# Performance work log

Hardware: AMD Instinct MI355X
Metric: run time of the kernel (lower is better)

Reference implementation:

```python
import jax, jax.numpy as jnp
import numpy as np
import math

D_MODEL = 1024
N_HEADS = 16
SEQ = 2048
BATCH = 2


def setup_inputs() -> dict:
    key = jax.random.key(0)
    ks = jax.random.split(key, 7)
    scale = 1.0 / math.sqrt(D_MODEL)
    return {
        "q": jax.random.normal(ks[0], (SEQ, BATCH, D_MODEL), jnp.float32),
        "k": jax.random.normal(ks[1], (SEQ, BATCH, D_MODEL), jnp.float32),
        "v": jax.random.normal(ks[2], (SEQ, BATCH, D_MODEL), jnp.float32),
        "in_proj_w": jax.random.normal(ks[3], (3 * D_MODEL, D_MODEL), jnp.float32) * scale,
        "in_proj_b": jax.random.normal(ks[4], (3 * D_MODEL,), jnp.float32) * 0.01,
        "out_proj_w": jax.random.normal(ks[5], (D_MODEL, D_MODEL), jnp.float32) * scale,
        "out_proj_b": jax.random.normal(ks[6], (D_MODEL,), jnp.float32) * 0.01,
    }


def reference(q, k, v, in_proj_w, in_proj_b, out_proj_w, out_proj_b):
    # q, k, v: (S, B, D) seq-first layout as in the torch module
    S, B, D = q.shape
    H = N_HEADS
    dk = D // H
    wq, wk, wv = jnp.split(in_proj_w, 3, axis=0)   # each (D, D)
    bq, bk, bv = jnp.split(in_proj_b, 3, axis=0)   # each (D,)
    qp = q @ wq.T + bq
    kp = k @ wk.T + bk
    vp = v @ wv.T + bv
    # (S, B, D) -> (S, B*H, dk) -> (B*H, S, dk)
    def to_heads(x, s):
        return x.reshape(s, B * H, dk).transpose(1, 0, 2)
    qh = to_heads(qp, S)
    kh = to_heads(kp, k.shape[0])
    vh = to_heads(vp, v.shape[0])
    # scores: (B*H, Sq, Sk)
    scores = jnp.einsum('bqd,bkd->bqk', qh, kh) / math.sqrt(dk)
    probs = jax.nn.softmax(scores, axis=-1)
    attn = jnp.einsum('bqk,bkd->bqd', probs, vh)   # (B*H, S, dk)
    # (B*H, S, dk) -> (S, B*H, dk) -> (S*B, D)
    attn = attn.transpose(1, 0, 2).reshape(S * B, D)
    out = attn @ out_proj_w.T + out_proj_b
    return out.reshape(S, B, D)
```

## Files before the change

kernel.cpp:

```cpp
#include <hip/hip_runtime.h>
#include <math.h>

#define SEQ    2048
#define BATCH  2
#define DMODEL 1024
#define NHEADS 16
#define DK     64

typedef __attribute__((ext_vector_type(8))) short  bf16x8;
typedef __attribute__((ext_vector_type(4))) float  f32x4;
typedef __attribute__((ext_vector_type(8))) unsigned short u16x8;

#define GLD16(gp, lp) __builtin_amdgcn_global_load_lds(                      \
    (__attribute__((address_space(1))) void*)(gp),                            \
    (__attribute__((address_space(3))) void*)(lp), 16, 0, 0)

__device__ inline unsigned short f2bf(float f) {
    unsigned int u = __float_as_uint(f);
    u += 0x7fffu + ((u >> 16) & 1u);
    return (unsigned short)(u >> 16);
}

__device__ inline unsigned int pk2bf(float a, float b) {
#if __has_builtin(__builtin_amdgcn_cvt_pk_bf16_f32)
    typedef __attribute__((ext_vector_type(2))) __bf16 v2bf;
    v2bf r = __builtin_amdgcn_cvt_pk_bf16_f32(a, b);
    unsigned int u; __builtin_memcpy(&u, &r, 4); return u;
#else
    return (unsigned int)f2bf(a) | ((unsigned int)f2bf(b) << 16);
#endif
}

__device__ inline float fast_exp2(float x) {
#if __has_builtin(__builtin_amdgcn_exp2f)
    return __builtin_amdgcn_exp2f(x);
#else
    return __expf(x * 0.69314718055994531f);
#endif
}

#define WS_QB   0u
#define WS_KB   4194304u
#define WS_VB   8388608u
#define WS_WIB  12582912u
#define WS_WOB  15728640u
#define WS_QH   16777216u
#define WS_KH   20971520u
#define WS_VT   25165824u
#define WS_ATT  29360128u

__global__ __launch_bounds__(256) void cast_all_kernel(
    const float* __restrict__ q, const float* __restrict__ k,
    const float* __restrict__ v, const float* __restrict__ w_in,
    const float* __restrict__ w_out, unsigned short* __restrict__ ws)
{
    const int gid = blockIdx.x * 256 + threadIdx.x;
    const float* src; unsigned short* dst;
    if (gid < 524288)       { int g = gid;           src = q     + (size_t)g*8; dst = ws + WS_QB  + (size_t)g*8; }
    else if (gid < 1048576) { int g = gid - 524288;  src = k     + (size_t)g*8; dst = ws + WS_KB  + (size_t)g*8; }
    else if (gid < 1572864) { int g = gid - 1048576; src = v     + (size_t)g*8; dst = ws + WS_VB  + (size_t)g*8; }
    else if (gid < 1966080) { int g = gid - 1572864; src = w_in  + (size_t)g*8; dst = ws + WS_WIB + (size_t)g*8; }
    else                    { int g = gid - 1966080; src = w_out + (size_t)g*8; dst = ws + WS_WOB + (size_t)g*8; }
    float4 a = *(const float4*)src;
    float4 b = *(const float4*)(src + 4);
    u16x8 o;
    o[0]=f2bf(a.x); o[1]=f2bf(a.y); o[2]=f2bf(a.z); o[3]=f2bf(a.w);
    o[4]=f2bf(b.x); o[5]=f2bf(b.y); o[6]=f2bf(b.z); o[7]=f2bf(b.w);
    *(u16x8*)dst = o;
}

__global__ __launch_bounds__(256) void qkv_gemm_kernel(
    const unsigned short* __restrict__ ws_in, const float* __restrict__ bias,
    unsigned short* __restrict__ ws_out)
{
    __shared__ unsigned short As[128*32];
    __shared__ unsigned short Bs[128*32];

    const int t    = threadIdx.x;
    const int lane = t & 63;
    const int w    = t >> 6;
    const int lrow = lane & 15;
    const int quad = lane >> 4;
    const int wm   = (w >> 1) * 64;
    const int wn   = (w & 1) * 64;

    const int n0    = blockIdx.x * 128;
    const int m0    = blockIdx.y * 128;
    const int which = n0 >> 10;

    const unsigned short* A = ws_in + WS_QB + (size_t)which * 4194304u;
    const unsigned short* B = ws_in + WS_WIB;

    const int srow = t >> 2;
    const int scc  = (t & 3) ^ ((t >> 3) & 3);
    const unsigned short* gA0 = A + (size_t)(m0 + srow) * 1024 + scc * 8;
    const unsigned short* gA1 = A + (size_t)(m0 + 64 + srow) * 1024 + scc * 8;
    const unsigned short* gB0 = B + (size_t)(n0 + srow) * 1024 + scc * 8;
    const unsigned short* gB1 = B + (size_t)(n0 + 64 + srow) * 1024 + scc * 8;

    f32x4 acc[4][4] = {};

    #pragma unroll 1
    for (int kt = 0; kt < 1024; kt += 32) {
        __syncthreads();
        GLD16(gA0, As + (size_t)t * 8);
        GLD16(gA1, As + (size_t)(t + 256) * 8);
        GLD16(gB0, Bs + (size_t)t * 8);
        GLD16(gB1, Bs + (size_t)(t + 256) * 8);
        gA0 += 32; gA1 += 32; gB0 += 32; gB1 += 32;
        __syncthreads();

        bf16x8 af[4], bf[4];
        #pragma unroll
        for (int mt = 0; mt < 4; ++mt) {
            const int r = wm + mt*16 + lrow;
            af[mt] = *(const bf16x8*)(As + r*32 + ((quad ^ ((r>>1)&3))*8));
        }
        #pragma unroll
        for (int nt = 0; nt < 4; ++nt) {
            const int r = wn + nt*16 + lrow;
            bf[nt] = *(const bf16x8*)(Bs + r*32 + ((quad ^ ((r>>1)&3))*8));
        }
        #pragma unroll
        for (int mt = 0; mt < 4; ++mt)
            #pragma unroll
            for (int nt = 0; nt < 4; ++nt)
                acc[mt][nt] = __builtin_amdgcn_mfma_f32_16x16x32_bf16(
                    af[mt], bf[nt], acc[mt][nt], 0, 0, 0);
    }

    unsigned short* dstQK = ws_out + WS_QH + (size_t)which * 4194304u;
    unsigned short* dstV  = ws_out + WS_VT;
    const float qscale = 0.18033688011112042f;

    #pragma unroll
    for (int nt = 0; nt < 4; ++nt) {
        const int n = n0 + wn + nt*16 + lrow;
        const float bn = bias[n];
        const int h = (n & 1023) >> 6;
        const int d = n & 63;
        #pragma unroll
        for (int mt = 0; mt < 4; ++mt) {
            if (which < 2) {
                #pragma unroll
                for (int r = 0; r < 4; ++r) {
                    const int m = m0 + wm + mt*16 + quad*4 + r;
                    const int s = m >> 1, b = m & 1;
                    float val = acc[mt][nt][r] + bn;
                    if (which == 0) val *= qscale;
                    dstQK[((size_t)((b<<4) + h) * 2048 + s) * 64 + d] = f2bf(val);
                }
            } else {
                const int m_base = m0 + wm + mt*16 + quad*4;
                const int s0 = m_base >> 1;
                unsigned int pk0 = pk2bf(acc[mt][nt][0] + bn, acc[mt][nt][2] + bn);
                unsigned int pk1 = pk2bf(acc[mt][nt][1] + bn, acc[mt][nt][3] + bn);
                *(unsigned int*)(dstV + ((size_t)h*64 + d)*2048 + s0)        = pk0;
                *(unsigned int*)(dstV + ((size_t)(16 + h)*64 + d)*2048 + s0) = pk1;
            }
        }
    }
}

__global__ __launch_bounds__(128) void attn_mfma_kernel(
    const unsigned short* __restrict__ qh, const unsigned short* __restrict__ kh,
    const unsigned short* __restrict__ vt, unsigned short* __restrict__ attn)
{
    __shared__ unsigned short Qs[64*64];
    __shared__ unsigned short Ks[64*64];
    __shared__ unsigned short Vts[64*64];
    __shared__ unsigned short Ps[64*64];

    const int t    = threadIdx.x;
    const int lane = t & 63;
    const int w    = t >> 6;
    const int lrow = lane & 15;
    const int quad = lane >> 4;

    const int qt = blockIdx.x;
    const int bh = blockIdx.y;

    const unsigned short* Qg = qh + ((size_t)bh * 2048 + qt * 64) * 64;
    const unsigned short* Kb = kh + (size_t)bh * 2048 * 64;
    const unsigned short* Vb = vt + (size_t)bh * 64 * 2048;

    #pragma unroll
    for (int i = 0; i < 4; ++i) {
        const int c = i*128 + t;
        const int row = c >> 3, cc = (c & 7) ^ (row & 7);
        GLD16(Qg + (size_t)row*64 + cc*8, Qs + (size_t)c*8);
    }

    f32x4 O[4][2] = {};
    float m_i[2] = {-INFINITY, -INFINITY}, l_i[2] = {0.f, 0.f};

    #pragma unroll 1
    for (int ktile = 0; ktile < 32; ++ktile) {
        __syncthreads();
        const unsigned short* Kg = Kb + (size_t)ktile * 64 * 64;
        const unsigned short* Vg = Vb + (size_t)ktile * 64;
        #pragma unroll
        for (int i = 0; i < 4; ++i) {
            const int c = i*128 + t;
            const int row = c >> 3, cc = (c & 7) ^ (row & 7);
            GLD16(Kg + (size_t)row*64   + cc*8, Ks  + (size_t)c*8);
            GLD16(Vg + (size_t)row*2048 + cc*8, Vts + (size_t)c*8);
        }
        __syncthreads();

        f32x4 ST[4][2] = {};
        #pragma unroll
        for (int kk = 0; kk < 2; ++kk) {
            bf16x8 kf[4], qf[2];
            #pragma unroll
            for (int m = 0; m < 4; ++m) {
                const int r = m*16 + lrow;
                kf[m] = *(const bf16x8*)(Ks + r*64 + (((kk*4+quad) ^ (r&7))*8));
            }
            #pragma unroll
            for (int n = 0; n < 2; ++n) {
                const int r = w*32 + n*16 + lrow;
                qf[n] = *(const bf16x8*)(Qs + r*64 + (((kk*4+quad) ^ (r&7))*8));
            }
            #pragma unroll
            for (int m = 0; m < 4; ++m)
                #pragma unroll
                for (int n = 0; n < 2; ++n)
                    ST[m][n] = __builtin_amdgcn_mfma_f32_16x16x32_bf16(
                        kf[m], qf[n], ST[m][n], 0, 0, 0);
        }

        float mx[2], al[2];
        int anynew = 0;
        #pragma unroll
        for (int n = 0; n < 2; ++n) {
            float mm;
            #pragma unroll
            for (int m = 0; m < 4; ++m) {
                float m01 = fmaxf(fmaxf(ST[m][n][0], ST[m][n][1]),
                                  fmaxf(ST[m][n][2], ST[m][n][3]));
                mm = (m == 0) ? m01 : fmaxf(mm, m01);
            }
            mm = fmaxf(mm, __shfl_xor(mm, 16, 64));
            mm = fmaxf(mm, __shfl_xor(mm, 32, 64));
            mx[n] = mm;
            anynew |= (mm > m_i[n]);
        }

        if (__any(anynew)) {
            #pragma unroll
            for (int n = 0; n < 2; ++n) {
                const float mn = fmaxf(m_i[n], mx[n]);
                al[n] = fast_exp2(m_i[n] - mn);
                m_i[n] = mn;
            }
            #pragma unroll
            for (int dt = 0; dt < 4; ++dt)
                #pragma unroll
                for (int n = 0; n < 2; ++n)
                    O[dt][n] *= al[n];
        } else {
            al[0] = 1.f; al[1] = 1.f;
        }

        #pragma unroll
        for (int n = 0; n < 2; ++n) {
            const int prow = w*32 + n*16 + lrow;
            const float mn = m_i[n];
            float rsum = 0.f;
            #pragma unroll
            for (int m = 0; m < 4; ++m) {
                const float p0 = fast_exp2(ST[m][n][0] - mn);
                const float p1 = fast_exp2(ST[m][n][1] - mn);
                const float p2 = fast_exp2(ST[m][n][2] - mn);
                const float p3 = fast_exp2(ST[m][n][3] - mn);
                rsum += (p0 + p1) + (p2 + p3);
                uint2 pk;
                pk.x = pk2bf(p0, p1);
                pk.y = pk2bf(p2, p3);
                const int sc = (m*2 + (quad >> 1)) ^ (prow & 7);
                *(uint2*)(Ps + prow*64 + sc*8 + (quad & 1)*4) = pk;
            }
            rsum += __shfl_xor(rsum, 16, 64);
            rsum += __shfl_xor(rsum, 32, 64);
            l_i[n] = l_i[n]*al[n] + rsum;
        }

        #pragma unroll
        for (int kk = 0; kk < 2; ++kk) {
            bf16x8 vf[4], pf[2];
            #pragma unroll
            for (int dt = 0; dt < 4; ++dt) {
                const int r = dt*16 + lrow;
                vf[dt] = *(const bf16x8*)(Vts + r*64 + (((kk*4+quad) ^ (r&7))*8));
            }
            #pragma unroll
            for (int n = 0; n < 2; ++n) {
                const int r = w*32 + n*16 + lrow;
                pf[n] = *(const bf16x8*)(Ps + r*64 + (((kk*4+quad) ^ (r&7))*8));
            }
            #pragma unroll
            for (int dt = 0; dt < 4; ++dt)
                #pragma unroll
                for (int n = 0; n < 2; ++n)
                    O[dt][n] = __builtin_amdgcn_mfma_f32_16x16x32_bf16(
                        vf[dt], pf[n], O[dt][n], 0, 0, 0);
        }
    }

    const int b_ = bh >> 4, h_ = bh & 15;
    #pragma unroll
    for (int n = 0; n < 2; ++n) {
        const float inv = 1.f / l_i[n];
        const int s_ = qt*64 + w*32 + n*16 + lrow;
        unsigned short* dst = attn + ((size_t)(s_*2 + b_)) * 1024 + h_*64;
        #pragma unroll
        for (int dt = 0; dt < 4; ++dt) {
            uint2 pk;
            pk.x = pk2bf(O[dt][n][0]*inv, O[dt][n][1]*inv);
            pk.y = pk2bf(O[dt][n][2]*inv, O[dt][n][3]*inv);
            *(uint2*)(dst + dt*16 + quad*4) = pk;
        }
    }
}

__global__ __launch_bounds__(256) void out_gemm_kernel(
    const unsigned short* __restrict__ A, const unsigned short* __restrict__ B,
    const float* __restrict__ bias, float* __restrict__ out)
{
    __shared__ unsigned short As[64*32];
    __shared__ unsigned short Bs[128*32];

    const int t    = threadIdx.x;
    const int lane = t & 63;
    const int w    = t >> 6;
    const int lrow = lane & 15;
    const int quad = lane >> 4;
    const int wn   = (w >> 1) * 64;
    const int wm   = (w & 1) * 32;

    const int n0 = blockIdx.x * 128;
    const int m0 = blockIdx.y * 64;

    const int srow = t >> 2;
    const int scc  = (t & 3) ^ ((t >> 3) & 3);
    const unsigned short* gA0 = A + (size_t)(m0 + srow) * 1024 + scc * 8;
    const unsigned short* gB0 = B + (size_t)(n0 + srow) * 1024 + scc * 8;
    const unsigned short* gB1 = B + (size_t)(n0 + 64 + srow) * 1024 + scc * 8;

    f32x4 acc[2][4] = {};

    #pragma unroll 1
    for (int kt = 0; kt < 1024; kt += 32) {
        __syncthreads();
        GLD16(gA0, As + (size_t)t * 8);
        GLD16(gB0, Bs + (size_t)t * 8);
        GLD16(gB1, Bs + (size_t)(t + 256) * 8);
        gA0 += 32; gB0 += 32; gB1 += 32;
        __syncthreads();

        bf16x8 af[2], bf[4];
        #pragma unroll
        for (int mt = 0; mt < 2; ++mt) {
            const int r = wm + mt*16 + lrow;
            af[mt] = *(const bf16x8*)(As + r*32 + ((quad ^ ((r>>1)&3))*8));
        }
        #pragma unroll
        for (int nt = 0; nt < 4; ++nt) {
            const int r = wn + nt*16 + lrow;
            bf[nt] = *(const bf16x8*)(Bs + r*32 + ((quad ^ ((r>>1)&3))*8));
        }
        #pragma unroll
        for (int mt = 0; mt < 2; ++mt)
            #pragma unroll
            for (int nt = 0; nt < 4; ++nt)
                acc[mt][nt] = __builtin_amdgcn_mfma_f32_16x16x32_bf16(
                    af[mt], bf[nt], acc[mt][nt], 0, 0, 0);
    }

    #pragma unroll
    for (int nt = 0; nt < 4; ++nt) {
        const int n = n0 + wn + nt*16 + lrow;
        const float bn = bias[n];
        #pragma unroll
        for (int mt = 0; mt < 2; ++mt) {
            #pragma unroll
            for (int r = 0; r < 4; ++r) {
                const int m = m0 + wm + mt*16 + quad*4 + r;
                out[(size_t)m * 1024 + n] = acc[mt][nt][r] + bn;
            }
        }
    }
}

extern "C" void kernel_launch(void* const* d_in, const int* in_sizes, int n_in,
                              void* d_out, int out_size, void* d_ws, size_t ws_size,
                              hipStream_t stream) {
    const float* q     = (const float*)d_in[0];
    const float* k     = (const float*)d_in[1];
    const float* v     = (const float*)d_in[2];
    const float* w_in  = (const float*)d_in[3];
    const float* b_in  = (const float*)d_in[4];
    const float* w_out = (const float*)d_in[5];
    const float* b_out = (const float*)d_in[6];
    float* out = (float*)d_out;

    unsigned short* ws = (unsigned short*)d_ws;

    cast_all_kernel<<<8192, 256, 0, stream>>>(q, k, v, w_in, w_out, ws);
    qkv_gemm_kernel<<<dim3(24, 32), 256, 0, stream>>>(ws, b_in, ws);
    attn_mfma_kernel<<<dim3(32, 32), 128, 0, stream>>>(
        ws + WS_QH, ws + WS_KH, ws + WS_VT, ws + WS_ATT);
    out_gemm_kernel<<<dim3(8, 64), 256, 0, stream>>>(
        ws + WS_ATT, ws + WS_WOB, b_out, out);
}
```

Baseline: 252.4 us.

## Compute softmax row sums via MFMA ones-row and use four waves per block

The attention kernel now launches 256 threads (four waves), each wave owning 16 query rows instead of 32. The shuffle-based row-sum reduction is replaced by an extra V tile row filled with bf16 1.0, so the P·V MFMA also accumulates the softmax denominator in a fifth accumulator. This removes per-tile shuffle reductions and halves per-wave register state, at the cost of one extra MFMA per k-step and lower K/V reuse per wave.

```diff
diff --git a/kernel.cpp b/kernel.cpp
--- a/kernel.cpp
+++ b/kernel.cpp
@@ -162,13 +162,13 @@
     }
 }
 
-__global__ __launch_bounds__(128) void attn_mfma_kernel(
+__global__ __launch_bounds__(256) void attn_mfma_kernel(
     const unsigned short* __restrict__ qh, const unsigned short* __restrict__ kh,
     const unsigned short* __restrict__ vt, unsigned short* __restrict__ attn)
 {
     __shared__ unsigned short Qs[64*64];
     __shared__ unsigned short Ks[64*64];
-    __shared__ unsigned short Vts[64*64];
+    __shared__ unsigned short Vts[80*64];
     __shared__ unsigned short Ps[64*64];
 
     const int t    = threadIdx.x;
@@ -185,14 +185,22 @@
     const unsigned short* Vb = vt + (size_t)bh * 64 * 2048;
 
     #pragma unroll
-    for (int i = 0; i < 4; ++i) {
-        const int c = i*128 + t;
+    for (int i = 0; i < 2; ++i) {
+        const int c = i*256 + t;
         const int row = c >> 3, cc = (c & 7) ^ (row & 7);
         GLD16(Qg + (size_t)row*64 + cc*8, Qs + (size_t)c*8);
     }
-
-    f32x4 O[4][2] = {};
-    float m_i[2] = {-INFINITY, -INFINITY}, l_i[2] = {0.f, 0.f};
+    if (t < 128) {
+        const int row = 64 + (t >> 3);
+        const unsigned short fill = (row == 64) ? (unsigned short)0x3F80 : (unsigned short)0;
+        u16x8 cv;
+        #pragma unroll
+        for (int j = 0; j < 8; ++j) cv[j] = fill;
+        *(u16x8*)(Vts + row*64 + (t & 7)*8) = cv;
+    }
+
+    f32x4 O[5] = {};
+    float m_i = -INFINITY;
 
     #pragma unroll 1
     for (int ktile = 0; ktile < 32; ++ktile) {
@@ -200,127 +208,82 @@
         const unsigned short* Kg = Kb + (size_t)ktile * 64 * 64;
         const unsigned short* Vg = Vb + (size_t)ktile * 64;
         #pragma unroll
-        for (int i = 0; i < 4; ++i) {
-            const int c = i*128 + t;
+        for (int i = 0; i < 2; ++i) {
+            const int c = i*256 + t;
             const int row = c >> 3, cc = (c & 7) ^ (row & 7);
             GLD16(Kg + (size_t)row*64   + cc*8, Ks  + (size_t)c*8);
             GLD16(Vg + (size_t)row*2048 + cc*8, Vts + (size_t)c*8);
         }
         __syncthreads();
 
-        f32x4 ST[4][2] = {};
+        f32x4 ST[4] = {};
         #pragma unroll
         for (int kk = 0; kk < 2; ++kk) {
-            bf16x8 kf[4], qf[2];
+            const int qr = w*16 + lrow;
+            bf16x8 qf = *(const bf16x8*)(Qs + qr*64 + (((kk*4+quad) ^ (qr&7))*8));
             #pragma unroll
             for (int m = 0; m < 4; ++m) {
                 const int r = m*16 + lrow;
-                kf[m] = *(const bf16x8*)(Ks + r*64 + (((kk*4+quad) ^ (r&7))*8));
+                bf16x8 kf = *(const bf16x8*)(Ks + r*64 + (((kk*4+quad) ^ (r&7))*8));
+                ST[m] = __builtin_amdgcn_mfma_f32_16x16x32_bf16(kf, qf, ST[m], 0, 0, 0);
             }
-            #pragma unroll
-            for (int n = 0; n < 2; ++n) {
-                const int r = w*32 + n*16 + lrow;
-                qf[n] = *(const bf16x8*)(Qs + r*64 + (((kk*4+quad) ^ (r&7))*8));
+        }
+
+        float mm = fmaxf(fmaxf(ST[0][0], ST[0][1]), fmaxf(ST[0][2], ST[0][3]));
+        #pragma unroll
+        for (int m = 1; m < 4; ++m)
+            mm = fmaxf(mm, fmaxf(fmaxf(ST[m][0], ST[m][1]),
+                                 fmaxf(ST[m][2], ST[m][3])));
+        mm = fmaxf(mm, __shfl_xor(mm, 16, 64));
+        mm = fmaxf(mm, __shfl_xor(mm, 32, 64));
+
+        if (__any(mm > m_i)) {
+            const float mn = fmaxf(m_i, mm);
+            const float al = fast_exp2(m_i - mn);
+            m_i = mn;
+            #pragma unroll
+            for (int d = 0; d < 5; ++d) O[d] *= al;
+        }
+
+        const int prow = w*16 + lrow;
+        #pragma unroll
+        for (int m = 0; m < 4; ++m) {
+            const float p0 = fast_exp2(ST[m][0] - m_i);
+            const float p1 = fast_exp2(ST[m][1] - m_i);
+            const float p2 = fast_exp2(ST[m][2] - m_i);
+            const float p3 = fast_exp2(ST[m][3] - m_i);
+            uint2 pk;
+            pk.x = pk2bf(p0, p1);
+            pk.y = pk2bf(p2, p3);
+            const int sc = (m*2 + (quad >> 1)) ^ (prow & 7);
+            *(uint2*)(Ps + prow*64 + sc*8 + (quad & 1)*4) = pk;
+        }
+
+        #pragma unroll
+        for (int kk = 0; kk < 2; ++kk) {
+            bf16x8 pf = *(const bf16x8*)(Ps + prow*64 + (((kk*4+quad) ^ (prow&7))*8));
+            #pragma unroll
+            for (int d = 0; d < 5; ++d) {
+                const int r = d*16 + lrow;
+                bf16x8 vf = *(const bf16x8*)(Vts + r*64 + (((kk*4+quad) ^ (r&7))*8));
+                O[d] = __builtin_amdgcn_mfma_f32_16x16x32_bf16(vf, pf, O[d], 0, 0, 0);
             }
-            #pragma unroll
-            for (int m = 0; m < 4; ++m)
-                #pragma unroll
-                for (int n = 0; n < 2; ++n)
-                    ST[m][n] = __builtin_amdgcn_mfma_f32_16x16x32_bf16(
-                        kf[m], qf[n], ST[m][n], 0, 0, 0);
-        }
-
-        float mx[2], al[2];
-        int anynew = 0;
-        #pragma unroll
-        for (int n = 0; n < 2; ++n) {
-            float mm;
-            #pragma unroll
-            for (int m = 0; m < 4; ++m) {
-                float m01 = fmaxf(fmaxf(ST[m][n][0], ST[m][n][1]),
-                                  fmaxf(ST[m][n][2], ST[m][n][3]));
-                mm = (m == 0) ? m01 : fmaxf(mm, m01);
-            }
-            mm = fmaxf(mm, __shfl_xor(mm, 16, 64));
-            mm = fmaxf(mm, __shfl_xor(mm, 32, 64));
-            mx[n] = mm;
-            anynew |= (mm > m_i[n]);
-        }
-
-        if (__any(anynew)) {
-            #pragma unroll
-            for (int n = 0; n < 2; ++n) {
-                const float mn = fmaxf(m_i[n], mx[n]);
-                al[n] = fast_exp2(m_i[n] - mn);
-                m_i[n] = mn;
-            }
-            #pragma unroll
-            for (int dt = 0; dt < 4; ++dt)
-                #pragma unroll
-                for (int n = 0; n < 2; ++n)
-                    O[dt][n] *= al[n];
-        } else {
-            al[0] = 1.f; al[1] = 1.f;
-        }
-
-        #pragma unroll
-        for (int n = 0; n < 2; ++n) {
-            const int prow = w*32 + n*16 + lrow;
-            const float mn = m_i[n];
-            float rsum = 0.f;
-            #pragma unroll
-            for (int m = 0; m < 4; ++m) {
-                const float p0 = fast_exp2(ST[m][n][0] - mn);
-                const float p1 = fast_exp2(ST[m][n][1] - mn);
-                const float p2 = fast_exp2(ST[m][n][2] - mn);
-                const float p3 = fast_exp2(ST[m][n][3] - mn);
-                rsum += (p0 + p1) + (p2 + p3);
-                uint2 pk;
-                pk.x = pk2bf(p0, p1);
-                pk.y = pk2bf(p2, p3);
-                const int sc = (m*2 + (quad >> 1)) ^ (prow & 7);
-                *(uint2*)(Ps + prow*64 + sc*8 + (quad & 1)*4) = pk;
-            }
-            rsum += __shfl_xor(rsum, 16, 64);
-            rsum += __shfl_xor(rsum, 32, 64);
-            l_i[n] = l_i[n]*al[n] + rsum;
-        }
-
-        #pragma unroll
-        for (int kk = 0; kk < 2; ++kk) {
-            bf16x8 vf[4], pf[2];
-            #pragma unroll
-            for (int dt = 0; dt < 4; ++dt) {
-                const int r = dt*16 + lrow;
-                vf[dt] = *(const bf16x8*)(Vts + r*64 + (((kk*4+quad) ^ (r&7))*8));
-            }
-            #pragma unroll
-            for (int n = 0; n < 2; ++n) {
-                const int r = w*32 + n*16 + lrow;
-                pf[n] = *(const bf16x8*)(Ps + r*64 + (((kk*4+quad) ^ (r&7))*8));
-            }
-            #pragma unroll
-            for (int dt = 0; dt < 4; ++dt)
-                #pragma unroll
-                for (int n = 0; n < 2; ++n)
-                    O[dt][n] = __builtin_amdgcn_mfma_f32_16x16x32_bf16(
-                        vf[dt], pf[n], O[dt][n], 0, 0, 0);
-        }
-    }
+        }
+    }
+
+    const float lv = O[4][0];
+    const float l  = __shfl(lv, lrow, 64);
+    const float inv = 1.f / l;
 
     const int b_ = bh >> 4, h_ = bh & 15;
+    const int s_ = qt*64 + w*16 + lrow;
+    unsigned short* dst = attn + ((size_t)(s_*2 + b_)) * 1024 + h_*64;
     #pragma unroll
-    for (int n = 0; n < 2; ++n) {
-        const float inv = 1.f / l_i[n];
-        const int s_ = qt*64 + w*32 + n*16 + lrow;
-        unsigned short* dst = attn + ((size_t)(s_*2 + b_)) * 1024 + h_*64;
-        #pragma unroll
-        for (int dt = 0; dt < 4; ++dt) {
-            uint2 pk;
-            pk.x = pk2bf(O[dt][n][0]*inv, O[dt][n][1]*inv);
-            pk.y = pk2bf(O[dt][n][2]*inv, O[dt][n][3]*inv);
-            *(uint2*)(dst + dt*16 + quad*4) = pk;
-        }
+    for (int dt = 0; dt < 4; ++dt) {
+        uint2 pk;
+        pk.x = pk2bf(O[dt][0]*inv, O[dt][1]*inv);
+        pk.y = pk2bf(O[dt][2]*inv, O[dt][3]*inv);
+        *(uint2*)(dst + dt*16 + quad*4) = pk;
     }
 }
 
@@ -409,7 +372,7 @@
 
     cast_all_kernel<<<8192, 256, 0, stream>>>(q, k, v, w_in, w_out, ws);
     qkv_gemm_kernel<<<dim3(24, 32), 256, 0, stream>>>(ws, b_in, ws);
-    attn_mfma_kernel<<<dim3(32, 32), 128, 0, stream>>>(
+    attn_mfma_kernel<<<dim3(32, 32), 256, 0, stream>>>(
         ws + WS_QH, ws + WS_KH, ws + WS_VT, ws + WS_ATT);
     out_gemm_kernel<<<dim3(8, 64), 256, 0, stream>>>(
         ws + WS_ATT, ws + WS_WOB, b_out, out);
```

Result: no change. 252.5 us (+0.0%).

## Enlarge attention Q tile to 128 rows and compute row sums via ones-row MFMA

Applied to the files above, without the earlier changes.

Each attention block now has 4 waves covering 128 query rows instead of 2 waves covering 64. Each K/V tile loaded into LDS is therefore shared by twice as many queries, which halves global K/V traffic per query. The softmax denominator is now computed by adding a constant row of ones (plus zero padding) to the V tile and running one extra MFMA column block. This replaces the per-tile cross-lane shuffle reductions, but costs about 25% more PV MFMA work and sums bf16-rounded probabilities. The grid halves to 512 blocks, which lowers the number of blocks per CU.

```diff
diff --git a/kernel.cpp b/kernel.cpp
--- a/kernel.cpp
+++ b/kernel.cpp
@@ -162,14 +162,14 @@
     }
 }
 
-__global__ __launch_bounds__(128) void attn_mfma_kernel(
+__global__ __launch_bounds__(256) void attn_mfma_kernel(
     const unsigned short* __restrict__ qh, const unsigned short* __restrict__ kh,
     const unsigned short* __restrict__ vt, unsigned short* __restrict__ attn)
 {
-    __shared__ unsigned short Qs[64*64];
+    __shared__ unsigned short Qs[128*64];
     __shared__ unsigned short Ks[64*64];
-    __shared__ unsigned short Vts[64*64];
-    __shared__ unsigned short Ps[64*64];
+    __shared__ unsigned short Vts[80*64];
+    __shared__ unsigned short Ps[128*64];
 
     const int t    = threadIdx.x;
     const int lane = t & 63;
@@ -180,19 +180,27 @@
     const int qt = blockIdx.x;
     const int bh = blockIdx.y;
 
-    const unsigned short* Qg = qh + ((size_t)bh * 2048 + qt * 64) * 64;
+    const unsigned short* Qg = qh + ((size_t)bh * 2048 + qt * 128) * 64;
     const unsigned short* Kb = kh + (size_t)bh * 2048 * 64;
     const unsigned short* Vb = vt + (size_t)bh * 64 * 2048;
 
     #pragma unroll
     for (int i = 0; i < 4; ++i) {
-        const int c = i*128 + t;
+        const int c = i*256 + t;
         const int row = c >> 3, cc = (c & 7) ^ (row & 7);
         GLD16(Qg + (size_t)row*64 + cc*8, Qs + (size_t)c*8);
     }
-
-    f32x4 O[4][2] = {};
-    float m_i[2] = {-INFINITY, -INFINITY}, l_i[2] = {0.f, 0.f};
+    if (t < 128) {
+        const int row = 64 + (t >> 3);
+        const unsigned short fill = (row == 64) ? (unsigned short)0x3F80 : (unsigned short)0;
+        u16x8 cv;
+        #pragma unroll
+        for (int j = 0; j < 8; ++j) cv[j] = fill;
+        *(u16x8*)(Vts + row*64 + (t & 7)*8) = cv;
+    }
+
+    f32x4 O[5][2] = {};
+    float m_i[2] = {-INFINITY, -INFINITY};
 
     #pragma unroll 1
     for (int ktile = 0; ktile < 32; ++ktile) {
@@ -200,8 +208,8 @@
         const unsigned short* Kg = Kb + (size_t)ktile * 64 * 64;
         const unsigned short* Vg = Vb + (size_t)ktile * 64;
         #pragma unroll
-        for (int i = 0; i < 4; ++i) {
-            const int c = i*128 + t;
+        for (int i = 0; i < 2; ++i) {
+            const int c = i*256 + t;
             const int row = c >> 3, cc = (c & 7) ^ (row & 7);
             GLD16(Kg + (size_t)row*64   + cc*8, Ks  + (size_t)c*8);
             GLD16(Vg + (size_t)row*2048 + cc*8, Vts + (size_t)c*8);
@@ -211,16 +219,16 @@
         f32x4 ST[4][2] = {};
         #pragma unroll
         for (int kk = 0; kk < 2; ++kk) {
-            bf16x8 kf[4], qf[2];
+            bf16x8 qf[2], kf[4];
+            #pragma unroll
+            for (int n = 0; n < 2; ++n) {
+                const int qr = w*32 + n*16 + lrow;
+                qf[n] = *(const bf16x8*)(Qs + qr*64 + (((kk*4+quad) ^ (qr&7))*8));
+            }
             #pragma unroll
             for (int m = 0; m < 4; ++m) {
                 const int r = m*16 + lrow;
                 kf[m] = *(const bf16x8*)(Ks + r*64 + (((kk*4+quad) ^ (r&7))*8));
-            }
-            #pragma unroll
-            for (int n = 0; n < 2; ++n) {
-                const int r = w*32 + n*16 + lrow;
-                qf[n] = *(const bf16x8*)(Qs + r*64 + (((kk*4+quad) ^ (r&7))*8));
             }
             #pragma unroll
             for (int m = 0; m < 4; ++m)
@@ -230,17 +238,16 @@
                         kf[m], qf[n], ST[m][n], 0, 0, 0);
         }
 
-        float mx[2], al[2];
+        float mx[2];
         int anynew = 0;
         #pragma unroll
         for (int n = 0; n < 2; ++n) {
-            float mm;
-            #pragma unroll
-            for (int m = 0; m < 4; ++m) {
-                float m01 = fmaxf(fmaxf(ST[m][n][0], ST[m][n][1]),
-                                  fmaxf(ST[m][n][2], ST[m][n][3]));
-                mm = (m == 0) ? m01 : fmaxf(mm, m01);
-            }
+            float mm = fmaxf(fmaxf(ST[0][n][0], ST[0][n][1]),
+                             fmaxf(ST[0][n][2], ST[0][n][3]));
+            #pragma unroll
+            for (int m = 1; m < 4; ++m)
+                mm = fmaxf(mm, fmaxf(fmaxf(ST[m][n][0], ST[m][n][1]),
+                                     fmaxf(ST[m][n][2], ST[m][n][3])));
             mm = fmaxf(mm, __shfl_xor(mm, 16, 64));
             mm = fmaxf(mm, __shfl_xor(mm, 32, 64));
             mx[n] = mm;
@@ -251,68 +258,59 @@
             #pragma unroll
             for (int n = 0; n < 2; ++n) {
                 const float mn = fmaxf(m_i[n], mx[n]);
-                al[n] = fast_exp2(m_i[n] - mn);
+                const float al = fast_exp2(m_i[n] - mn);
                 m_i[n] = mn;
-            }
-            #pragma unroll
-            for (int dt = 0; dt < 4; ++dt)
                 #pragma unroll
-                for (int n = 0; n < 2; ++n)
-                    O[dt][n] *= al[n];
-        } else {
-            al[0] = 1.f; al[1] = 1.f;
+                for (int d = 0; d < 5; ++d) O[d][n] *= al;
+            }
         }
 
         #pragma unroll
         for (int n = 0; n < 2; ++n) {
             const int prow = w*32 + n*16 + lrow;
             const float mn = m_i[n];
-            float rsum = 0.f;
             #pragma unroll
             for (int m = 0; m < 4; ++m) {
                 const float p0 = fast_exp2(ST[m][n][0] - mn);
                 const float p1 = fast_exp2(ST[m][n][1] - mn);
                 const float p2 = fast_exp2(ST[m][n][2] - mn);
                 const float p3 = fast_exp2(ST[m][n][3] - mn);
-                rsum += (p0 + p1) + (p2 + p3);
                 uint2 pk;
                 pk.x = pk2bf(p0, p1);
                 pk.y = pk2bf(p2, p3);
                 const int sc = (m*2 + (quad >> 1)) ^ (prow & 7);
                 *(uint2*)(Ps + prow*64 + sc*8 + (quad & 1)*4) = pk;
             }
-            rsum += __shfl_xor(rsum, 16, 64);
-            rsum += __shfl_xor(rsum, 32, 64);
-            l_i[n] = l_i[n]*al[n] + rsum;
         }
 
         #pragma unroll
         for (int kk = 0; kk < 2; ++kk) {
-            bf16x8 vf[4], pf[2];
-            #pragma unroll
-            for (int dt = 0; dt < 4; ++dt) {
-                const int r = dt*16 + lrow;
-                vf[dt] = *(const bf16x8*)(Vts + r*64 + (((kk*4+quad) ^ (r&7))*8));
-            }
+            bf16x8 pf[2], vf[5];
             #pragma unroll
             for (int n = 0; n < 2; ++n) {
-                const int r = w*32 + n*16 + lrow;
-                pf[n] = *(const bf16x8*)(Ps + r*64 + (((kk*4+quad) ^ (r&7))*8));
-            }
-            #pragma unroll
-            for (int dt = 0; dt < 4; ++dt)
+                const int prow = w*32 + n*16 + lrow;
+                pf[n] = *(const bf16x8*)(Ps + prow*64 + (((kk*4+quad) ^ (prow&7))*8));
+            }
+            #pragma unroll
+            for (int d = 0; d < 5; ++d) {
+                const int r = d*16 + lrow;
+                vf[d] = *(const bf16x8*)(Vts + r*64 + (((kk*4+quad) ^ (r&7))*8));
+            }
+            #pragma unroll
+            for (int d = 0; d < 5; ++d)
                 #pragma unroll
                 for (int n = 0; n < 2; ++n)
-                    O[dt][n] = __builtin_amdgcn_mfma_f32_16x16x32_bf16(
-                        vf[dt], pf[n], O[dt][n], 0, 0, 0);
+                    O[d][n] = __builtin_amdgcn_mfma_f32_16x16x32_bf16(
+                        vf[d], pf[n], O[d][n], 0, 0, 0);
         }
     }
 
     const int b_ = bh >> 4, h_ = bh & 15;
     #pragma unroll
     for (int n = 0; n < 2; ++n) {
-        const float inv = 1.f / l_i[n];
-        const int s_ = qt*64 + w*32 + n*16 + lrow;
+        const float l  = __shfl(O[4][n][0], lrow, 64);
+        const float inv = 1.f / l;
+        const int s_ = qt*128 + w*32 + n*16 + lrow;
         unsigned short* dst = attn + ((size_t)(s_*2 + b_)) * 1024 + h_*64;
         #pragma unroll
         for (int dt = 0; dt < 4; ++dt) {
@@ -409,7 +407,7 @@
 
     cast_all_kernel<<<8192, 256, 0, stream>>>(q, k, v, w_in, w_out, ws);
     qkv_gemm_kernel<<<dim3(24, 32), 256, 0, stream>>>(ws, b_in, ws);
-    attn_mfma_kernel<<<dim3(32, 32), 128, 0, stream>>>(
+    attn_mfma_kernel<<<dim3(16, 32), 256, 0, stream>>>(
         ws + WS_QH, ws + WS_KH, ws + WS_VT, ws + WS_ATT);
     out_gemm_kernel<<<dim3(8, 64), 256, 0, stream>>>(
         ws + WS_ATT, ws + WS_WOB, b_out, out);
```

After: 252.9 us. Within noise of the previous version (+0.2%).
